# Kernel optimization log

Hardware: AMD Instinct MI355X
Metric: run time of the kernel (lower is better)

Reference implementation:

```python
import jax, jax.numpy as jnp
import numpy as np

EPS = 1e-7  # keras backend.epsilon()
NUM_ROUTING = 3


def squash(v, axis=-1):
    s2 = jnp.sum(jnp.square(v), axis=axis, keepdims=True)
    scale = s2 / (1.0 + s2) / jnp.sqrt(s2 + EPS)
    return scale * v


def setup_inputs() -> dict:
    key = jax.random.key(0)
    k1, k2 = jax.random.split(key)
    B, J, I, P, Q = 64, 32, 2048, 32, 16
    inputs = jax.random.normal(k1, (B, I, Q), dtype=jnp.float32)
    # glorot_uniform for W [J, I, P, Q]
    fan_in, fan_out = Q, P
    limit = np.sqrt(6.0 / (fan_in + fan_out))
    W = jax.random.uniform(k2, (J, I, P, Q), dtype=jnp.float32, minval=-limit, maxval=limit)
    return {"inputs": inputs, "W": W}


def reference(inputs, W):
    # prediction vectors: u_hat[b,j,i,p] = sum_q inputs[b,i,q] * W[j,i,p,q]
    inputs_hat = jnp.einsum('biq,jipq->bjip', inputs, W)  # [B,J,I,P]
    inputs_hat_stop = jax.lax.stop_gradient(inputs_hat)
    B, J, I, _ = inputs_hat.shape
    b = jnp.zeros((B, J, I), dtype=inputs_hat.dtype)
    for _ in range(NUM_ROUTING - 1):
        c = jax.nn.softmax(b, axis=1)  # softmax over output capsules j
        v = squash(jnp.einsum('bji,bjip->bjp', c, inputs_hat_stop))
        b = b + jnp.einsum('bjp,bjip->bji', v, inputs_hat_stop)
    c = jax.nn.softmax(b, axis=1)
    return squash(jnp.einsum('bji,bjip->bjp', c, inputs_hat))  # [B,J,P]
```

## Files before the change

kernel.cpp:

```cpp
#include <hip/hip_runtime.h>


namespace {

using bfrag = __attribute__((ext_vector_type(8))) short;
using ffrag = __attribute__((ext_vector_type(4))) float;

constexpr int I_DIM = 2048;
constexpr int B_DIM = 64;
constexpr int N_DIM = 1024;
constexpr int TI    = 16;

__device__ __forceinline__ unsigned short f2bf(float f) {
    unsigned int u = __float_as_uint(f);
    return (unsigned short)((u + 0x7fffu + ((u >> 16) & 1u)) >> 16);
}

template<int CTRL>
__device__ __forceinline__ float dppf(float x) {
    return __int_as_float(
        __builtin_amdgcn_update_dpp(0, __float_as_int(x), CTRL, 0xF, 0xF, true));
}
__device__ __forceinline__ float sum16(float x) {
    x += dppf<0x121>(x); x += dppf<0x122>(x);
    x += dppf<0x124>(x); x += dppf<0x128>(x);
    return x;
}
__device__ __forceinline__ float max16(float x) {
    x = fmaxf(x, dppf<0x121>(x)); x = fmaxf(x, dppf<0x122>(x));
    x = fmaxf(x, dppf<0x124>(x)); x = fmaxf(x, dppf<0x128>(x));
    return x;
}

__device__ __forceinline__ void gl2lds16(const void* gsrc, void* ldst) {
    __builtin_amdgcn_global_load_lds(
        (const __attribute__((address_space(1))) void*)gsrc,
        (__attribute__((address_space(3))) void*)ldst, 16, 0, 0);
}

__device__ __forceinline__ void barrier_lgkm() {
    asm volatile("s_waitcnt lgkmcnt(0)" ::: "memory");
    __builtin_amdgcn_s_barrier();
    __builtin_amdgcn_sched_barrier(0);
}


__global__ __launch_bounds__(256)
void conv_w(const float* __restrict__ W, unsigned short* __restrict__ Wt) {
    const int t = blockIdx.x * 256 + threadIdx.x;
    const int i = t >> 10, n = t & 1023;
    const float* src = W + ((((n >> 5) * I_DIM + i) * 32 + (n & 31)) << 4);
    unsigned int o[8];
    #pragma unroll
    for (int k = 0; k < 8; ++k)
        o[k] = (unsigned int)f2bf(src[2 * k]) | ((unsigned int)f2bf(src[2 * k + 1]) << 16);
    uint4* d0 = reinterpret_cast<uint4*>(Wt + (((size_t)i * 2 + 0) * 1024 + n) * 8);
    uint4* d1 = reinterpret_cast<uint4*>(Wt + (((size_t)i * 2 + 1) * 1024 + n) * 8);
    *d0 = make_uint4(o[0], o[1], o[2], o[3]);
    *d1 = make_uint4(o[4], o[5], o[6], o[7]);
}

__global__ __launch_bounds__(256)
void conv_x(const float* __restrict__ x, unsigned short* __restrict__ xT2) {
    const int t = blockIdx.x * 256 + threadIdx.x;
    const int i = t >> 6, b = t & 63;
    const float* src = x + (((size_t)b * I_DIM + i) << 4);
    unsigned int o[16];
    #pragma unroll
    for (int k = 0; k < 8; ++k) {
        const float f0 = src[2 * k], f1 = src[2 * k + 1];
        const unsigned short h0 = f2bf(f0), h1 = f2bf(f1);
        const float l0 = f0 - __uint_as_float(((unsigned int)h0) << 16);
        const float l1 = f1 - __uint_as_float(((unsigned int)h1) << 16);
        o[k]     = (unsigned int)h0       | ((unsigned int)h1 << 16);
        o[8 + k] = (unsigned int)f2bf(l0) | ((unsigned int)f2bf(l1) << 16);
    }
    #pragma unroll
    for (int g = 0; g < 4; ++g) {
        uint4* dst = reinterpret_cast<uint4*>(xT2 + (((size_t)i * 4 + g) * 64 + b) * 8);
        *dst = make_uint4(o[4 * g], o[4 * g + 1], o[4 * g + 2], o[4 * g + 3]);
    }
}

#define WAITC() do { if (w == 7) asm volatile("s_waitcnt vmcnt(5)" ::: "memory"); \
                     else        asm volatile("s_waitcnt vmcnt(4)" ::: "memory"); } while (0)

template<int ROUTED>
__global__ __launch_bounds__(512, 2)
void caps_fused(const unsigned short* __restrict__ Wt,
                const unsigned short* __restrict__ xT2,
                const float* __restrict__ v_in,
                float* __restrict__ s_out)
{
    __shared__ short wbuf[2][16384];
    __shared__ short xbuf[2][512];
    __shared__ float d_buf[16 * 36];
    __shared__ float c_buf[16 * 36];

    const int tid = threadIdx.x;
    const int w   = tid >> 6;
    const int l   = tid & 63;
    const int g   = l >> 4;
    const int li  = l & 15;
    const int j0  = w << 2;

    const int bid = (int)blockIdx.x;
    const int V   = (bid & 7) * 64 + (bid >> 3);
    const int it  = V >> 2;
    const int b0  = (V & 3) << 4;
    const int i0  = it * TI;

    float vr[4][8];
    if (ROUTED) {
        #pragma unroll
        for (int r = 0; r < 4; ++r)
            #pragma unroll
            for (int t = 0; t < 8; ++t)
                vr[r][t] = v_in[((b0 + (g << 2) + r) * 32 + j0 + (t >> 1)) * 32
                                + ((t & 1) << 4) + li];
        asm volatile("s_waitcnt vmcnt(0)" ::: "memory");
    }

    auto stage = [&](int i, int bufn) {
        const unsigned short* wsrc = Wt + ((size_t)i << 14);
        #pragma unroll
        for (int k = 0; k < 4; ++k) {
            const int c = (w << 2) + k;
            gl2lds16(wsrc + (c << 9) + (l << 3), &wbuf[bufn][c << 9]);
        }
        if (w == 7)
            gl2lds16(xT2 + (((size_t)i << 2) + (l >> 4)) * 512 + ((b0 + (l & 15)) << 3),
                     &xbuf[bufn][0]);
    };

    stage(i0, 0);
    stage(i0 + 1, 1);
    WAITC();
    __builtin_amdgcn_s_barrier();
    __builtin_amdgcn_sched_barrier(0);

    ffrag s[8];
    #pragma unroll
    for (int t = 0; t < 8; ++t) s[t] = ffrag{0.f, 0.f, 0.f, 0.f};

    for (int ii = 0; ii < TI; ++ii) {
        const int cur = ii & 1;

        const bfrag a = *reinterpret_cast<const bfrag*>(&xbuf[cur][((g << 4) + li) << 3]);
        ffrag u[8];
        #pragma unroll
        for (int t = 0; t < 8; ++t) {
            const int n0 = ((j0 + (t >> 1)) << 5) + ((t & 1) << 4);
            const bfrag bt = *reinterpret_cast<const bfrag*>(
                &wbuf[cur][((g & 1) << 13) + ((n0 + li) << 3)]);
            if (ROUTED) {
                ffrag z{0.f, 0.f, 0.f, 0.f};
                u[t] = __builtin_amdgcn_mfma_f32_16x16x32_bf16(a, bt, z, 0, 0, 0);
            } else {
                s[t] = __builtin_amdgcn_mfma_f32_16x16x32_bf16(a, bt, s[t], 0, 0, 0);
            }
        }

        if (ROUTED) {
            #pragma unroll
            for (int r = 0; r < 4; ++r) {
                float d0 = u[0][r] * vr[r][0] + u[1][r] * vr[r][1];
                float d1 = u[2][r] * vr[r][2] + u[3][r] * vr[r][3];
                float d2 = u[4][r] * vr[r][4] + u[5][r] * vr[r][5];
                float d3 = u[6][r] * vr[r][6] + u[7][r] * vr[r][7];
                d0 = sum16(d0); d1 = sum16(d1); d2 = sum16(d2); d3 = sum16(d3);
                float sel = d0;
                sel = (li == 1) ? d1 : sel;
                sel = (li == 2) ? d2 : sel;
                sel = (li == 3) ? d3 : sel;
                if (li < 4) d_buf[((g << 2) + r) * 36 + j0 + li] = sel;
            }
        }
        barrier_lgkm();

        if (ii + 2 < TI) stage(i0 + ii + 2, cur);

        if (ROUTED) {
            const int row = (w << 1) + (l >> 5), jx = l & 31;
            const float dv = d_buf[row * 36 + jx];
            float m = max16(dv);
            m = fmaxf(m, __shfl_xor(m, 16));
            const float e = __expf(dv - m);
            float sm = sum16(e);
            sm += __shfl_xor(sm, 16);
            c_buf[row * 36 + jx] = e / sm;
            barrier_lgkm();

            #pragma unroll
            for (int r = 0; r < 4; ++r) {
                const ffrag cr = *reinterpret_cast<const ffrag*>(
                    &c_buf[((g << 2) + r) * 36 + j0]);
                #pragma unroll
                for (int t = 0; t < 8; ++t)
                    s[t][r] += cr[t >> 1] * u[t][r];
            }
        }

        if (ii + 2 < TI) WAITC();
        else             asm volatile("s_waitcnt vmcnt(0)" ::: "memory");
        __builtin_amdgcn_s_barrier();
        __builtin_amdgcn_sched_barrier(0);
    }

    const float sc = ROUTED ? 1.f : (1.f / 32.f);
    #pragma unroll
    for (int t = 0; t < 8; ++t) {
        const int n0 = ((j0 + (t >> 1)) << 5) + ((t & 1) << 4);
        #pragma unroll
        for (int r = 0; r < 4; ++r)
            atomicAdd(&s_out[(size_t)(b0 + (g << 2) + r) * N_DIM + n0 + li],
                      s[t][r] * sc);
    }
}

__global__ __launch_bounds__(256)
void squash_add(const float* __restrict__ s, const float* __restrict__ base,
                float* __restrict__ dst) {
    const int t = blockIdx.x * 256 + threadIdx.x;
    if (t >= B_DIM * 32) return;
    const float* sp = s + t * 32;
    float n2 = 0.f;
    #pragma unroll
    for (int p = 0; p < 32; ++p) { const float xv = sp[p]; n2 += xv * xv; }
    const float scl = n2 / ((1.f + n2) * sqrtf(n2 + 1e-7f));
    float* op = dst + t * 32;
    #pragma unroll
    for (int p = 0; p < 32; ++p)
        op[p] = (base ? base[t * 32 + p] : 0.f) + scl * sp[p];
}

}

extern "C" void kernel_launch(void* const* d_in, const int* in_sizes, int n_in,
                              void* d_out, int out_size, void* d_ws, size_t ws_size,
                              hipStream_t stream) {
    const float* x = (const float*)d_in[0];
    const float* W = (const float*)d_in[1];
    float* out = (float*)d_out;

    const size_t needW = (size_t)I_DIM * 2 * 1024 * 8 * 2;
    const size_t needX = (size_t)I_DIM * 4 * 64 * 8 * 2;
    const size_t needS = (size_t)B_DIM * N_DIM * 4;

    char* pp = (char*)d_ws;
    unsigned short* Wt  = (unsigned short*)pp; pp += needW;
    unsigned short* xT2 = (unsigned short*)pp; pp += needX;
    float* s  = (float*)pp; pp += needS;
    float* v1 = (float*)pp; pp += needS;
    float* vs = (float*)pp;
    (void)ws_size;

    conv_x<<<(I_DIM * B_DIM) / 256, 256, 0, stream>>>(x, xT2);
    conv_w<<<(I_DIM * N_DIM) / 256, 256, 0, stream>>>(W, Wt);

    const dim3 rg(512), rb(512);

    hipMemsetAsync(s, 0, needS, stream);
    caps_fused<0><<<rg, rb, 0, stream>>>(Wt, xT2, nullptr, s);
    squash_add<<<8, 256, 0, stream>>>(s, nullptr, v1);

    hipMemsetAsync(s, 0, needS, stream);
    caps_fused<1><<<rg, rb, 0, stream>>>(Wt, xT2, v1, s);
    squash_add<<<8, 256, 0, stream>>>(s, v1, vs);

    hipMemsetAsync(s, 0, needS, stream);
    caps_fused<1><<<rg, rb, 0, stream>>>(Wt, xT2, vs, s);
    squash_add<<<8, 256, 0, stream>>>(s, nullptr, out);
}
```

Baseline: 286.5 us.

## Fuse W conversion into first pass, drop LDS staging, replace atomics with partial-sum reduce

Removes the separate conv_w kernel: the first routing pass reads fp32 W directly, converts it to bf16 with a packed convert instruction, feeds the MFMA and writes the bf16 copy for later passes. The routed passes drop LDS double buffering and load B fragments directly from global memory into registers. They recompute u with a second MFMA instead of keeping it live, and store v_in packed as bf16 to cut register use so occupancy can rise to 4 blocks. Atomic accumulation and the memsets give way to per-tile partial sums plus a reduction kernel. This writes and reads a 32 MB partial buffer per pass and loses the explicit prefetch.

```diff
diff --git a/kernel.cpp b/kernel.cpp
--- a/kernel.cpp
+++ b/kernel.cpp
@@ -10,11 +10,19 @@
 constexpr int B_DIM = 64;
 constexpr int N_DIM = 1024;
 constexpr int TI    = 16;
+constexpr int NIT   = I_DIM / TI;
 
 __device__ __forceinline__ unsigned short f2bf(float f) {
     unsigned int u = __float_as_uint(f);
     return (unsigned short)((u + 0x7fffu + ((u >> 16) & 1u)) >> 16);
 }
+__device__ __forceinline__ unsigned int cvtpk(float lo, float hi) {
+    unsigned int r;
+    asm("v_cvt_pk_bf16_f32 %0, %1, %2" : "=v"(r) : "v"(lo), "v"(hi));
+    return r;
+}
+__device__ __forceinline__ float bflo(unsigned int u) { return __uint_as_float(u << 16); }
+__device__ __forceinline__ float bfhi(unsigned int u) { return __uint_as_float(u & 0xffff0000u); }
 
 template<int CTRL>
 __device__ __forceinline__ float dppf(float x) {
@@ -31,33 +39,10 @@
     x = fmaxf(x, dppf<0x124>(x)); x = fmaxf(x, dppf<0x128>(x));
     return x;
 }
-
-__device__ __forceinline__ void gl2lds16(const void* gsrc, void* ldst) {
-    __builtin_amdgcn_global_load_lds(
-        (const __attribute__((address_space(1))) void*)gsrc,
-        (__attribute__((address_space(3))) void*)ldst, 16, 0, 0);
-}
-
 __device__ __forceinline__ void barrier_lgkm() {
     asm volatile("s_waitcnt lgkmcnt(0)" ::: "memory");
     __builtin_amdgcn_s_barrier();
     __builtin_amdgcn_sched_barrier(0);
-}
-
-
-__global__ __launch_bounds__(256)
-void conv_w(const float* __restrict__ W, unsigned short* __restrict__ Wt) {
-    const int t = blockIdx.x * 256 + threadIdx.x;
-    const int i = t >> 10, n = t & 1023;
-    const float* src = W + ((((n >> 5) * I_DIM + i) * 32 + (n & 31)) << 4);
-    unsigned int o[8];
-    #pragma unroll
-    for (int k = 0; k < 8; ++k)
-        o[k] = (unsigned int)f2bf(src[2 * k]) | ((unsigned int)f2bf(src[2 * k + 1]) << 16);
-    uint4* d0 = reinterpret_cast<uint4*>(Wt + (((size_t)i * 2 + 0) * 1024 + n) * 8);
-    uint4* d1 = reinterpret_cast<uint4*>(Wt + (((size_t)i * 2 + 1) * 1024 + n) * 8);
-    *d0 = make_uint4(o[0], o[1], o[2], o[3]);
-    *d1 = make_uint4(o[4], o[5], o[6], o[7]);
 }
 
 __global__ __launch_bounds__(256)
@@ -82,18 +67,15 @@
     }
 }
 
-#define WAITC() do { if (w == 7) asm volatile("s_waitcnt vmcnt(5)" ::: "memory"); \
-                     else        asm volatile("s_waitcnt vmcnt(4)" ::: "memory"); } while (0)
-
 template<int ROUTED>
-__global__ __launch_bounds__(512, 2)
-void caps_fused(const unsigned short* __restrict__ Wt,
+__global__ __launch_bounds__(512, 4)
+void caps_pass3(const float* __restrict__ Wf,
+                unsigned short* __restrict__ Wt_out,
+                const unsigned short* __restrict__ Wt,
                 const unsigned short* __restrict__ xT2,
                 const float* __restrict__ v_in,
-                float* __restrict__ s_out)
+                float* __restrict__ sp_out)
 {
-    __shared__ short wbuf[2][16384];
-    __shared__ short xbuf[2][512];
     __shared__ float d_buf[16 * 36];
     __shared__ float c_buf[16 * 36];
 
@@ -103,108 +85,110 @@
     const int g   = l >> 4;
     const int li  = l & 15;
     const int j0  = w << 2;
+    const int qb  = (g & 1) << 3;
 
     const int bid = (int)blockIdx.x;
-    const int V   = (bid & 7) * 64 + (bid >> 3);
+    const int V   = ((bid & 7) << 6) | (bid >> 3);
     const int it  = V >> 2;
-    const int b0  = (V & 3) << 4;
-    const int i0  = it * TI;
-
-    float vr[4][8];
+    const int bg  = V & 3;
+    const int b0  = bg << 4;
+    const int i0  = it << 4;
+
+    unsigned int vr[4][4];
     if (ROUTED) {
         #pragma unroll
         for (int r = 0; r < 4; ++r)
             #pragma unroll
+            for (int jj = 0; jj < 4; ++jj) {
+                const float* vp = v_in + (((b0 + (g << 2) + r) << 5) + j0 + jj) * 32;
+                vr[r][jj] = cvtpk(vp[li], vp[li + 16]);
+            }
+    }
+
+    ffrag s[8];
+    #pragma unroll
+    for (int t = 0; t < 8; ++t) s[t] = ffrag{0.f, 0.f, 0.f, 0.f};
+
+    for (int ii = 0; ii < TI; ++ii) {
+        const int i = i0 + ii;
+        const bfrag A0 = *reinterpret_cast<const bfrag*>(
+            xT2 + ((size_t)i << 11) + (g << 9) + ((b0 + li) << 3));
+
+        if constexpr (!ROUTED) {
+            #pragma unroll
+            for (int t = 0; t < 8; ++t) {
+                const int jj = t >> 1, ph = t & 1;
+                const float* wp = Wf + ((size_t)(j0 + jj) * I_DIM + i) * 512
+                                     + ((ph << 4) + li) * 16 + qb;
+                const float4 wa = *reinterpret_cast<const float4*>(wp);
+                const float4 wb = *reinterpret_cast<const float4*>(wp + 4);
+                union { uint4 u; bfrag b; } cv;
+                cv.u = make_uint4(cvtpk(wa.x, wa.y), cvtpk(wa.z, wa.w),
+                                  cvtpk(wb.x, wb.y), cvtpk(wb.z, wb.w));
+                if (bg == 0 && g < 2)
+                    *reinterpret_cast<bfrag*>(
+                        Wt_out + ((size_t)i << 14) + ((g & 1) << 13)
+                               + ((((j0 + jj) << 5) + (ph << 4) + li) << 3)) = cv.b;
+                s[t] = __builtin_amdgcn_mfma_f32_16x16x32_bf16(A0, cv.b, s[t], 0, 0, 0);
+            }
+        } else {
+            const unsigned short* xb = Wt + ((size_t)i << 14) + ((g & 1) << 13);
+            bfrag B[8];
+            #pragma unroll
             for (int t = 0; t < 8; ++t)
-                vr[r][t] = v_in[((b0 + (g << 2) + r) * 32 + j0 + (t >> 1)) * 32
-                                + ((t & 1) << 4) + li];
-        asm volatile("s_waitcnt vmcnt(0)" ::: "memory");
-    }
-
-    auto stage = [&](int i, int bufn) {
-        const unsigned short* wsrc = Wt + ((size_t)i << 14);
-        #pragma unroll
-        for (int k = 0; k < 4; ++k) {
-            const int c = (w << 2) + k;
-            gl2lds16(wsrc + (c << 9) + (l << 3), &wbuf[bufn][c << 9]);
+                B[t] = *reinterpret_cast<const bfrag*>(
+                    xb + ((((j0 + (t >> 1)) << 5) + ((t & 1) << 4) + li) << 3));
+
+            const ffrag z{0.f, 0.f, 0.f, 0.f};
+            ffrag u[8];
+            #pragma unroll
+            for (int t = 0; t < 8; ++t)
+                u[t] = __builtin_amdgcn_mfma_f32_16x16x32_bf16(A0, B[t], z, 0, 0, 0);
+
+            float dd[4][4];
+            #pragma unroll
+            for (int r = 0; r < 4; ++r)
+                #pragma unroll
+                for (int jj = 0; jj < 4; ++jj) {
+                    const unsigned int v2 = vr[r][jj];
+                    dd[r][jj] = sum16(u[2 * jj][r] * bflo(v2)
+                                    + u[2 * jj + 1][r] * bfhi(v2));
+                }
+            #pragma unroll
+            for (int r = 0; r < 4; ++r) {
+                float sel = dd[r][0];
+                sel = (li == 1) ? dd[r][1] : sel;
+                sel = (li == 2) ? dd[r][2] : sel;
+                sel = (li == 3) ? dd[r][3] : sel;
+                if (li < 4) d_buf[((g << 2) + r) * 36 + j0 + li] = sel;
+            }
+            barrier_lgkm();
+
+            {
+                const int row = tid >> 5, jx = tid & 31;
+                const float dv = d_buf[row * 36 + jx];
+                float m = max16(dv);
+                m = fmaxf(m, __shfl_xor(m, 16));
+                const float e = __expf(dv - m);
+                float sm = sum16(e);
+                sm += __shfl_xor(sm, 16);
+                c_buf[row * 36 + jx] = e / sm;
+            }
+            barrier_lgkm();
+
+            ffrag c4[4];
+            #pragma unroll
+            for (int r = 0; r < 4; ++r)
+                c4[r] = *reinterpret_cast<const ffrag*>(
+                    &c_buf[((g << 2) + r) * 36 + j0]);
+            #pragma unroll
+            for (int t = 0; t < 8; ++t) {
+                const ffrag u2 = __builtin_amdgcn_mfma_f32_16x16x32_bf16(A0, B[t], z, 0, 0, 0);
+                #pragma unroll
+                for (int r = 0; r < 4; ++r)
+                    s[t][r] += c4[r][t >> 1] * u2[r];
+            }
         }
-        if (w == 7)
-            gl2lds16(xT2 + (((size_t)i << 2) + (l >> 4)) * 512 + ((b0 + (l & 15)) << 3),
-                     &xbuf[bufn][0]);
-    };
-
-    stage(i0, 0);
-    stage(i0 + 1, 1);
-    WAITC();
-    __builtin_amdgcn_s_barrier();
-    __builtin_amdgcn_sched_barrier(0);
-
-    ffrag s[8];
-    #pragma unroll
-    for (int t = 0; t < 8; ++t) s[t] = ffrag{0.f, 0.f, 0.f, 0.f};
-
-    for (int ii = 0; ii < TI; ++ii) {
-        const int cur = ii & 1;
-
-        const bfrag a = *reinterpret_cast<const bfrag*>(&xbuf[cur][((g << 4) + li) << 3]);
-        ffrag u[8];
-        #pragma unroll
-        for (int t = 0; t < 8; ++t) {
-            const int n0 = ((j0 + (t >> 1)) << 5) + ((t & 1) << 4);
-            const bfrag bt = *reinterpret_cast<const bfrag*>(
-                &wbuf[cur][((g & 1) << 13) + ((n0 + li) << 3)]);
-            if (ROUTED) {
-                ffrag z{0.f, 0.f, 0.f, 0.f};
-                u[t] = __builtin_amdgcn_mfma_f32_16x16x32_bf16(a, bt, z, 0, 0, 0);
-            } else {
-                s[t] = __builtin_amdgcn_mfma_f32_16x16x32_bf16(a, bt, s[t], 0, 0, 0);
-            }
-        }
-
-        if (ROUTED) {
-            #pragma unroll
-            for (int r = 0; r < 4; ++r) {
-                float d0 = u[0][r] * vr[r][0] + u[1][r] * vr[r][1];
-                float d1 = u[2][r] * vr[r][2] + u[3][r] * vr[r][3];
-                float d2 = u[4][r] * vr[r][4] + u[5][r] * vr[r][5];
-                float d3 = u[6][r] * vr[r][6] + u[7][r] * vr[r][7];
-                d0 = sum16(d0); d1 = sum16(d1); d2 = sum16(d2); d3 = sum16(d3);
-                float sel = d0;
-                sel = (li == 1) ? d1 : sel;
-                sel = (li == 2) ? d2 : sel;
-                sel = (li == 3) ? d3 : sel;
-                if (li < 4) d_buf[((g << 2) + r) * 36 + j0 + li] = sel;
-            }
-        }
-        barrier_lgkm();
-
-        if (ii + 2 < TI) stage(i0 + ii + 2, cur);
-
-        if (ROUTED) {
-            const int row = (w << 1) + (l >> 5), jx = l & 31;
-            const float dv = d_buf[row * 36 + jx];
-            float m = max16(dv);
-            m = fmaxf(m, __shfl_xor(m, 16));
-            const float e = __expf(dv - m);
-            float sm = sum16(e);
-            sm += __shfl_xor(sm, 16);
-            c_buf[row * 36 + jx] = e / sm;
-            barrier_lgkm();
-
-            #pragma unroll
-            for (int r = 0; r < 4; ++r) {
-                const ffrag cr = *reinterpret_cast<const ffrag*>(
-                    &c_buf[((g << 2) + r) * 36 + j0]);
-                #pragma unroll
-                for (int t = 0; t < 8; ++t)
-                    s[t][r] += cr[t >> 1] * u[t][r];
-            }
-        }
-
-        if (ii + 2 < TI) WAITC();
-        else             asm volatile("s_waitcnt vmcnt(0)" ::: "memory");
-        __builtin_amdgcn_s_barrier();
-        __builtin_amdgcn_sched_barrier(0);
     }
 
     const float sc = ROUTED ? 1.f : (1.f / 32.f);
@@ -213,25 +197,33 @@
         const int n0 = ((j0 + (t >> 1)) << 5) + ((t & 1) << 4);
         #pragma unroll
         for (int r = 0; r < 4; ++r)
-            atomicAdd(&s_out[(size_t)(b0 + (g << 2) + r) * N_DIM + n0 + li],
-                      s[t][r] * sc);
+            sp_out[(((size_t)(it << 6) + b0 + (g << 2) + r) << 10) + n0 + li]
+                = s[t][r] * sc;
     }
 }
 
 __global__ __launch_bounds__(256)
-void squash_add(const float* __restrict__ s, const float* __restrict__ base,
-                float* __restrict__ dst) {
-    const int t = blockIdx.x * 256 + threadIdx.x;
-    if (t >= B_DIM * 32) return;
-    const float* sp = s + t * 32;
-    float n2 = 0.f;
-    #pragma unroll
-    for (int p = 0; p < 32; ++p) { const float xv = sp[p]; n2 += xv * xv; }
+void squash_reduce(const float* __restrict__ s_part,
+                   const float* __restrict__ base,
+                   float* __restrict__ dst) {
+    const int tid = threadIdx.x;
+    const int rr  = blockIdx.x * 8 + (tid >> 5);
+    const int p   = tid & 31;
+    const int b   = rr >> 5, jx = rr & 31;
+    const float* sp = s_part + (size_t)b * N_DIM + (jx << 5) + p;
+    float a0 = 0.f, a1 = 0.f, a2 = 0.f, a3 = 0.f;
+    for (int it2 = 0; it2 < NIT; it2 += 4) {
+        a0 += sp[(size_t)(it2 + 0) << 16];
+        a1 += sp[(size_t)(it2 + 1) << 16];
+        a2 += sp[(size_t)(it2 + 2) << 16];
+        a3 += sp[(size_t)(it2 + 3) << 16];
+    }
+    const float sv = (a0 + a1) + (a2 + a3);
+    float n2 = sv * sv;
+    n2 = sum16(n2);
+    n2 += __shfl_xor(n2, 16);
     const float scl = n2 / ((1.f + n2) * sqrtf(n2 + 1e-7f));
-    float* op = dst + t * 32;
-    #pragma unroll
-    for (int p = 0; p < 32; ++p)
-        op[p] = (base ? base[t * 32 + p] : 0.f) + scl * sp[p];
+    dst[rr * 32 + p] = (base ? base[rr * 32 + p] : 0.f) + scl * sv;
 }
 
 }
@@ -245,30 +237,28 @@
 
     const size_t needW = (size_t)I_DIM * 2 * 1024 * 8 * 2;
     const size_t needX = (size_t)I_DIM * 4 * 64 * 8 * 2;
-    const size_t needS = (size_t)B_DIM * N_DIM * 4;
+    const size_t needP = (size_t)NIT * B_DIM * N_DIM * 4;
+    const size_t needV = (size_t)B_DIM * N_DIM * 4;
 
     char* pp = (char*)d_ws;
     unsigned short* Wt  = (unsigned short*)pp; pp += needW;
     unsigned short* xT2 = (unsigned short*)pp; pp += needX;
-    float* s  = (float*)pp; pp += needS;
-    float* v1 = (float*)pp; pp += needS;
-    float* vs = (float*)pp;
+    float* s_part = (float*)pp; pp += needP;
+    float* v1     = (float*)pp; pp += needV;
+    float* vs     = (float*)pp;
     (void)ws_size;
 
     conv_x<<<(I_DIM * B_DIM) / 256, 256, 0, stream>>>(x, xT2);
-    conv_w<<<(I_DIM * N_DIM) / 256, 256, 0, stream>>>(W, Wt);
 
     const dim3 rg(512), rb(512);
-
-    hipMemsetAsync(s, 0, needS, stream);
-    caps_fused<0><<<rg, rb, 0, stream>>>(Wt, xT2, nullptr, s);
-    squash_add<<<8, 256, 0, stream>>>(s, nullptr, v1);
-
-    hipMemsetAsync(s, 0, needS, stream);
-    caps_fused<1><<<rg, rb, 0, stream>>>(Wt, xT2, v1, s);
-    squash_add<<<8, 256, 0, stream>>>(s, v1, vs);
-
-    hipMemsetAsync(s, 0, needS, stream);
-    caps_fused<1><<<rg, rb, 0, stream>>>(Wt, xT2, vs, s);
-    squash_add<<<8, 256, 0, stream>>>(s, nullptr, out);
-}
+    const dim3 qg(256), qb(256);
+
+    caps_pass3<0><<<rg, rb, 0, stream>>>(W, Wt, nullptr, xT2, nullptr, s_part);
+    squash_reduce<<<qg, qb, 0, stream>>>(s_part, nullptr, v1);
+
+    caps_pass3<1><<<rg, rb, 0, stream>>>(nullptr, nullptr, Wt, xT2, v1, s_part);
+    squash_reduce<<<qg, qb, 0, stream>>>(s_part, v1, vs);
+
+    caps_pass3<1><<<rg, rb, 0, stream>>>(nullptr, nullptr, Wt, xT2, vs, s_part);
+    squash_reduce<<<qg, qb, 0, stream>>>(s_part, nullptr, out);
+}
```

New measurement: 468.3 us. +63.5%, slower.
